# Kernel tuning notes

Hardware: AMD Instinct MI355X
Metric: run time of the kernel (lower is better)

## Reference

```python
import jax, jax.numpy as jnp
import numpy as np
from jax import lax


def conv1x1(x, w, b=None):
    # x: [B,C,H,W], w: [O,C]
    y = jnp.einsum('bchw,oc->bohw', x, w)
    if b is not None:
        y = y + b[None, :, None, None]
    return y


def conv1x9(x, w, b):
    # x: [B,C,H,W], w: [O,I,1,9], pad (0,4) -> same spatial size
    y = lax.conv_general_dilated(x, w, window_strides=(1, 1),
                                 padding=((0, 0), (4, 4)),
                                 dimension_numbers=('NCHW', 'OIHW', 'NCHW'))
    return y + b[None, :, None, None]


def skn(inputs, fc1_w, fc2_w):
    # Selective Kernel fusion: M=len(inputs), each [B,C,H,W]
    M = len(inputs)
    B, C = inputs[0].shape[0], inputs[0].shape[1]
    U = inputs[0]
    for t in inputs[1:]:
        U = U + t
    s = U.mean(axis=(2, 3))                               # [B,C] global avg pool
    z = jax.nn.leaky_relu(jnp.einsum('bc,oc->bo', s, fc1_w), 0.01)
    ab = jnp.einsum('bo,po->bp', z, fc2_w).reshape(B, M, C)
    a = jax.nn.softmax(ab, axis=1)                        # softmax over branches
    out = inputs[0] * a[:, 0][:, :, None, None]
    for i in range(1, M):
        out = out + inputs[i] * a[:, i][:, :, None, None]
    return out


def setup_inputs() -> dict:
    key = jax.random.key(0)
    ks = jax.random.split(key, 24)
    B, C, H, W = 2, 128, 128, 512
    Ch = C // 2
    p = lambda k, shp: (jax.random.normal(k, shp, jnp.float32) * 0.02)
    d = {}
    d['left_feat'] = jax.random.normal(ks[0], (B, C, H, W), jnp.float32)
    d['right_feat'] = jax.random.normal(ks[1], (B, C, H, W), jnp.float32)
    d['emb_l_w'] = p(ks[2], (Ch, C)); d['emb_l_b'] = p(ks[3], (Ch,))
    d['emb_r_w'] = p(ks[4], (Ch, C)); d['emb_r_b'] = p(ks[5], (Ch,))
    d['emb_lv_w'] = p(ks[6], (Ch, C)); d['emb_lv_b'] = p(ks[7], (Ch,))
    d['emb_rv_w'] = p(ks[8], (Ch, C)); d['emb_rv_b'] = p(ks[9], (Ch,))
    d['out_l_w'] = p(ks[10], (C, Ch)); d['out_l_b'] = p(ks[11], (C,))
    d['head_w'] = p(ks[12], (C, 2 * C)); d['head_b'] = p(ks[13], (C,))
    d['body_w1'] = p(ks[14], (3, C, C, 1, 9)); d['body_b1'] = p(ks[15], (3, C))
    d['body_w2'] = p(ks[16], (3, C, C, 1, 9)); d['body_b2'] = p(ks[17], (3, C))
    d['skn1_fc1_w'] = p(ks[18], (C // 4, C)); d['skn1_fc2_w'] = p(ks[19], (3 * C, C // 4))
    d['skn2_fc1_w'] = p(ks[20], (C // 4, C)); d['skn2_fc2_w'] = p(ks[21], (3 * C, C // 4))
    d['num_window'] = 4
    return d


def reference(left_feat, right_feat, emb_l_w, emb_l_b, emb_r_w, emb_r_b,
              emb_lv_w, emb_lv_b, emb_rv_w, emb_rv_b, out_l_w, out_l_b,
              head_w, head_b, body_w1, body_b1, body_w2, body_b2,
              skn1_fc1_w, skn1_fc2_w, skn2_fc1_w, skn2_fc2_w, num_window):
    B, C, H, W = left_feat.shape
    Ch = C // 2
    nw = int(num_window)
    win = W // nw

    Q = conv1x1(left_feat, emb_l_w, emb_l_b)     # [B,Ch,H,W]
    K = conv1x1(right_feat, emb_r_w, emb_r_b)
    V_left = conv1x1(left_feat, emb_lv_w, emb_lv_b)   # computed but unused (source bug)
    V_right = conv1x1(right_feat, emb_rv_w, emb_rv_b)

    # windowed per-row cross attention over width
    Qw = Q.transpose(0, 2, 3, 1).reshape(B, H, nw, win, Ch)   # [B,H,n,q,c]
    Kw = K.transpose(0, 2, 3, 1).reshape(B, H, nw, win, Ch)   # [B,H,n,k,c]
    Vr = V_right.transpose(0, 2, 3, 1).reshape(B, H, nw, win, Ch)

    score = jnp.einsum('bhnqc,bhnkc->bhnqk', Qw, Kw)          # [B,H,n,q,k]
    M_r2l = jax.nn.softmax(score, axis=-1)
    out = jnp.einsum('bhnqk,bhnkc->bhnqc', M_r2l, Vr)         # [B,H,n,q,c]
    warped = out.reshape(B, H, W, Ch).transpose(0, 3, 1, 2)   # [B,Ch,H,W]
    left_feat_warped = jax.nn.relu(conv1x1(warped, out_l_w, out_l_b))
    # NOTE: source code (num_window>1 branch) reuses M_right_to_left and V_right
    # for the right warp as well -> right_feat_warped == left_feat_warped.
    right_feat_warped = left_feat_warped

    # head conv + 3 residual blocks (1x9 convs)
    mixed = jax.nn.relu(conv1x1(jnp.concatenate([left_feat, right_feat], axis=1),
                                head_w, head_b))
    x = mixed
    for i in range(3):
        r = jax.nn.relu(conv1x9(x, body_w1[i], body_b1[i]))
        r = conv1x9(r, body_w2[i], body_b2[i])
        x = x + r
    mixed_feat = x

    left_out = skn([left_feat, left_feat_warped, mixed_feat], skn1_fc1_w, skn1_fc2_w)
    right_out = skn([right_feat, right_feat_warped, mixed_feat], skn2_fc1_w, skn2_fc2_w)
    return (left_out, right_out)
```

## Files before the change

kernel.cpp:

```cpp
#include <hip/hip_runtime.h>
#include <hip/hip_bf16.h>

typedef __attribute__((ext_vector_type(8))) short bf16x8;
typedef __attribute__((ext_vector_type(4))) float f32x4;
typedef unsigned short u16;
typedef unsigned int u32;

#define DI __device__ __forceinline__
#define MFMA16(a, b, c) __builtin_amdgcn_mfma_f32_16x16x32_bf16((a), (b), (c), 0, 0, 0)

constexpr int Hh = 128, Ww = 512;
constexpr int HW = 65536;
constexpr long FULL = 16777216;
constexpr long HALF = 8388608;

__device__ __align__(16) u16 g_buf[2 * FULL];
__device__ __align__(16) u16 g_w[950272];
__device__ __align__(16) float g_bias[1216];
__device__ __align__(16) float g_fc[32768];
__device__ __align__(16) float g_pools[1024];
__device__ __align__(16) float g_gates[1536];
__device__ __align__(16) float g_ppart[524288];
__device__ int g_flag;

constexpr int EMB_L = 0, EMB_R = 8192, EMB_RV = 16384, HEAD = 24576, OUTL = 57344, BODY = 65536;
constexpr int B_EMBL = 0, B_EMBR = 64, B_EMBRV = 128, B_OUTL = 192, B_HEAD = 320, B_B1 = 448, B_B2 = 832;
constexpr int FC1A = 0, FC2A = 4096, FC1B = 16384, FC2B = 20480;

DI float b2f(u16 u) { union { u32 i; float f; } v; v.i = (u32)u << 16; return v.f; }
DI u16 f2b(float f) {
  union { float fl; u32 u; } v; v.fl = f;
  return (u16)((v.u + 0x7FFFu + ((v.u >> 16) & 1u)) >> 16);
}
DI float ldf(const void* p, long i, int f) {
  return f ? ((const float*)p)[i] : b2f(((const u16*)p)[i]);
}
DI bf16x8 ld8(const void* p) { return *reinterpret_cast<const bf16x8*>(p); }
DI void gload16(const u16* src, char* lds_dst) {
  __builtin_amdgcn_global_load_lds(
      (const __attribute__((address_space(1))) void*)src,
      (__attribute__((address_space(3))) void*)lds_dst, 16, 0, 0);
}

__global__ void k_detect(const void* left) {
  if (threadIdx.x != 0 || blockIdx.x != 0) return;
  const u16* pu = (const u16*)left;
  int okb = 0;
  for (int i = 0; i < 256; i++) {
    float x = b2f(pu[i]);
    float a = fabsf(x);
    if (x == 0.f || (a > 1e-8f && a < 1e4f)) okb++;
  }
  g_flag = (okb >= 230) ? 0 : 1;
}

__global__ void k_pack(const void* w1, const void* w2, const void* embl, const void* embr,
                       const void* embrv, const void* outl, const void* head,
                       const void* embl_b, const void* embr_b, const void* embrv_b,
                       const void* outl_b, const void* head_b, const void* b1, const void* b2,
                       const void* f1a, const void* f2a, const void* f1b, const void* f2b_) {
  int f = g_flag;
  int i = blockIdx.x * 256 + threadIdx.x;
  int job = blockIdx.y;
  if (job == 0) {
    if (i >= 884736) return;
    int c = i & 127, o = (i >> 7) & 127;
    int rest = i >> 14;
    int t = rest % 9, bc = rest / 9;
    const void* src = (bc & 1) ? w2 : w1;
    int blk = bc >> 1;
    g_w[BODY + i] = f2b(ldf(src, (((long)(blk * 128 + o) * 128 + c)) * 9 + t, f));
  } else if (job == 1) {
    if (i >= 65536) return;
    float v;
    if (i < 8192) v = ldf(embl, i, f);
    else if (i < 16384) v = ldf(embr, i - 8192, f);
    else if (i < 24576) v = ldf(embrv, i - 16384, f);
    else if (i < 57344) v = ldf(head, i - 24576, f);
    else v = ldf(outl, i - 57344, f);
    g_w[i] = f2b(v);
  } else if (job == 2) {
    if (i >= 1216) return;
    float v;
    if (i < 64) v = ldf(embl_b, i, f);
    else if (i < 128) v = ldf(embr_b, i - 64, f);
    else if (i < 192) v = ldf(embrv_b, i - 128, f);
    else if (i < 320) v = ldf(outl_b, i - 192, f);
    else if (i < 448) v = ldf(head_b, i - 320, f);
    else if (i < 832) v = ldf(b1, i - 448, f);
    else v = ldf(b2, i - 832, f);
    g_bias[i] = v;
  } else {
    if (i >= 32768) return;
    float v;
    if (i < 4096) v = ldf(f1a, i, f);
    else if (i < 16384) v = ldf(f2a, i - 4096, f);
    else if (i < 20480) v = ldf(f1b, i - 16384, f);
    else v = ldf(f2b_, i - 20480, f);
    g_fc[i] = v;
  }
}

__global__ __launch_bounds__(256) void k_nchw2nhwc(const void* srcL, const void* srcR,
                                                   u16* __restrict__ dstL, u16* __restrict__ dstR) {
  __shared__ u16 tile[64][130];
  int f = g_flag;
  int w0 = blockIdx.x * 64;
  int h = blockIdx.y;
  int b = blockIdx.z & 1;
  int img = blockIdx.z >> 1;
  const void* src = img ? srcR : srcL;
  u16* dst = img ? dstR : dstL;
  int t = threadIdx.x;
  int wq = (t & 31) * 2, cb = t >> 5;
  for (int c0 = 0; c0 < 128; c0 += 8) {
    int c = c0 + cb;
    long base = (long)(b * 128 + c) * HW + h * Ww + w0 + wq;
    if (f) {
      float2 v = *reinterpret_cast<const float2*>((const float*)src + base);
      tile[wq][c] = f2b(v.x);
      tile[wq + 1][c] = f2b(v.y);
    } else {
      u32 v = *reinterpret_cast<const u32*>((const u16*)src + base);
      tile[wq][c] = (u16)v;
      tile[wq + 1][c] = (u16)(v >> 16);
    }
  }
  __syncthreads();
  int c = t & 127, wb = t >> 7;
  long obase = (long)b * HW + (long)h * Ww + w0;
  for (int w1i = 0; w1i < 64; w1i += 2) {
    int w = w1i + wb;
    dst[(obase + w) * 128 + c] = tile[w][c];
  }
  if (t < 128) {
    float s = 0.f;
#pragma unroll
    for (int w = 0; w < 64; w++) s += b2f(tile[w][t]);
    g_ppart[((img * 2 + b) * 128 + t) * 1024 + (h * 8 + blockIdx.x)] = s;
  }
}

template<int K, int N, bool RELU, bool NCHW_OUT>
__global__ __launch_bounds__(256) void k_gemm1x1(const u16* __restrict__ xt, const u16* __restrict__ w,
                                                 const float* __restrict__ bias, u16* __restrict__ out,
                                                 int wstride) {
  extern __shared__ __align__(16) char smem[];
  constexpr int SLOTS = (K * 2) / 16;
  constexpr int RB = K * 2;
  int t = threadIdx.x;
  long p0 = (long)blockIdx.x * 128;
  for (int u = t; u < 128 * SLOTS; u += 256) {
    int row = u / SLOTS, slot = u % SLOTS;
    int4 v = *reinterpret_cast<const int4*>(xt + (p0 + row) * K + slot * 8);
    *reinterpret_cast<int4*>(smem + (((u32)(row * RB + slot * 16)) ^ ((row & 7) << 4))) = v;
  }
  __syncthreads();
  int wid = t >> 6, lane = t & 63, l15 = lane & 15, l4 = lane >> 4;
  constexpr int WAVES_M = (N == 64) ? 4 : 2;
  constexpr int MF = (128 / WAVES_M) / 16;
  int wm = (N == 64) ? wid : (wid >> 1);
  int wn = (N == 64) ? 0 : (wid & 1);
  int prow0 = wm * (128 / WAVES_M);
  int ocol0 = wn * 64;
  f32x4 zz = {0.f, 0.f, 0.f, 0.f};
  f32x4 acc[MF][4];
#pragma unroll
  for (int m = 0; m < MF; m++)
#pragma unroll
    for (int n = 0; n < 4; n++) acc[m][n] = zz;
#pragma unroll
  for (int k0 = 0; k0 < K; k0 += 32) {
    bf16x8 a[MF], bw[4];
#pragma unroll
    for (int m = 0; m < MF; m++) {
      int row = prow0 + m * 16 + l15;
      a[m] = ld8(smem + (((u32)(row * RB + (k0 + l4 * 8) * 2)) ^ ((row & 7) << 4)));
    }
#pragma unroll
    for (int n = 0; n < 4; n++) {
      int o = ocol0 + n * 16 + l15;
      bw[n] = ld8(w + (long)o * wstride + k0 + l4 * 8);
    }
#pragma unroll
    for (int m = 0; m < MF; m++)
#pragma unroll
      for (int n = 0; n < 4; n++) acc[m][n] = MFMA16(a[m], bw[n], acc[m][n]);
  }
  if constexpr (!NCHW_OUT) {
#pragma unroll
    for (int m = 0; m < MF; m++)
#pragma unroll
      for (int n = 0; n < 4; n++) {
        int o = ocol0 + n * 16 + l15;
        float bb = bias[o];
#pragma unroll
        for (int r = 0; r < 4; r++) {
          long p = p0 + prow0 + m * 16 + l4 * 4 + r;
          float v = acc[m][n][r] + bb;
          if (RELU) v = fmaxf(v, 0.f);
          out[p * N + o] = f2b(v);
        }
      }
  } else {
    __syncthreads();
    u16* tb = reinterpret_cast<u16*>(smem) + wid * (64 * 66);
#pragma unroll
    for (int m = 0; m < MF; m++)
#pragma unroll
      for (int n = 0; n < 4; n++) {
        float bb = bias[ocol0 + n * 16 + l15];
#pragma unroll
        for (int r = 0; r < 4; r++) {
          int pl = m * 16 + l4 * 4 + r;
          float v = acc[m][n][r] + bb;
          if (RELU) v = fmaxf(v, 0.f);
          tb[(n * 16 + l15) * 66 + pl] = f2b(v);
        }
      }
    __syncthreads();
    int bq = (int)(p0 / HW);
    int rem = (int)(p0 % HW);
    int hq = rem / Ww, wq0 = rem % Ww;
    for (int o = 0; o < 64; o++) {
      out[((long)(bq * 128 + ocol0 + o)) * HW + hq * Ww + wq0 + prow0 + lane] = tb[o * 66 + lane];
    }
  }
}

__global__ __launch_bounds__(256) void k_emb3(const u16* __restrict__ leftT, const u16* __restrict__ rightT,
                                              const u16* __restrict__ gw, const float* __restrict__ gbias,
                                              u16* __restrict__ QT, u16* __restrict__ KT, u16* __restrict__ VrT) {
  extern __shared__ __align__(16) char smem[];
  int br = blockIdx.y;
  const u16* xt = (br == 0) ? leftT : rightT;
  const u16* w = gw + ((br == 0) ? EMB_L : (br == 1) ? EMB_R : EMB_RV);
  const float* bias = gbias + ((br == 0) ? B_EMBL : (br == 1) ? B_EMBR : B_EMBRV);
  u16* out = (br == 0) ? QT : (br == 1) ? KT : VrT;
  int t = threadIdx.x;
  long p0 = (long)blockIdx.x * 128;
  for (int u = t; u < 2048; u += 256) {
    int row = u >> 4, slot = u & 15;
    int4 v = *reinterpret_cast<const int4*>(xt + (p0 + row) * 128 + slot * 8);
    *reinterpret_cast<int4*>(smem + (((u32)(row * 256 + slot * 16)) ^ ((row & 7) << 4))) = v;
  }
  __syncthreads();
  int wid = t >> 6, lane = t & 63, l15 = lane & 15, l4 = lane >> 4;
  int prow0 = wid * 32;
  f32x4 zz = {0.f, 0.f, 0.f, 0.f};
  f32x4 acc[2][4];
#pragma unroll
  for (int m = 0; m < 2; m++)
#pragma unroll
    for (int n = 0; n < 4; n++) acc[m][n] = zz;
#pragma unroll
  for (int k0 = 0; k0 < 128; k0 += 32) {
    bf16x8 a[2], bw[4];
#pragma unroll
    for (int m = 0; m < 2; m++) {
      int row = prow0 + m * 16 + l15;
      a[m] = ld8(smem + (((u32)(row * 256 + (k0 + l4 * 8) * 2)) ^ ((row & 7) << 4)));
    }
#pragma unroll
    for (int n = 0; n < 4; n++) {
      int o = n * 16 + l15;
      bw[n] = ld8(w + (long)o * 128 + k0 + l4 * 8);
    }
#pragma unroll
    for (int m = 0; m < 2; m++)
#pragma unroll
      for (int n = 0; n < 4; n++) acc[m][n] = MFMA16(a[m], bw[n], acc[m][n]);
  }
#pragma unroll
  for (int m = 0; m < 2; m++)
#pragma unroll
    for (int n = 0; n < 4; n++) {
      int o = n * 16 + l15;
      float bb = bias[o];
#pragma unroll
      for (int r = 0; r < 4; r++) {
        long p = p0 + prow0 + m * 16 + l4 * 4 + r;
        out[p * 64 + o] = f2b(acc[m][n][r] + bb);
      }
    }
}

__global__ __launch_bounds__(256) void k_head(const u16* lt, const u16* rt,
                                              const u16* __restrict__ wh, const float* __restrict__ bh,
                                              u16* out) {
  extern __shared__ __align__(16) char smem[];
  int t = threadIdx.x;
  long p0 = (long)blockIdx.x * 128;
  for (int u = t; u < 2048; u += 256) {
    int row = u >> 4, slot = u & 15;
    u32 db = ((u32)(row * 256 + slot * 16)) ^ ((row & 7) << 4);
    *reinterpret_cast<int4*>(smem + db) = *reinterpret_cast<const int4*>(lt + (p0 + row) * 128 + slot * 8);
    *reinterpret_cast<int4*>(smem + 32768 + db) = *reinterpret_cast<const int4*>(rt + (p0 + row) * 128 + slot * 8);
  }
  __syncthreads();
  int wid = t >> 6, lane = t & 63, l15 = lane & 15, l4 = lane >> 4;
  int prow0 = (wid >> 1) * 64, ocol0 = (wid & 1) * 64;
  f32x4 zz = {0.f, 0.f, 0.f, 0.f};
  f32x4 acc[4][4];
#pragma unroll
  for (int m = 0; m < 4; m++)
#pragma unroll
    for (int n = 0; n < 4; n++) acc[m][n] = zz;
#pragma unroll
  for (int kk = 0; kk < 8; kk++) {
    int k0 = kk * 32;
    const char* sb = smem + ((kk >= 4) ? 32768 : 0);
    int kl = k0 & 127;
    bf16x8 a[4], bw[4];
#pragma unroll
    for (int m = 0; m < 4; m++) {
      int row = prow0 + m * 16 + l15;
      a[m] = ld8(sb + (((u32)(row * 256 + (kl + l4 * 8) * 2)) ^ ((row & 7) << 4)));
    }
#pragma unroll
    for (int n = 0; n < 4; n++) {
      int o = ocol0 + n * 16 + l15;
      bw[n] = ld8(wh + o * 256 + k0 + l4 * 8);
    }
#pragma unroll
    for (int m = 0; m < 4; m++)
#pragma unroll
      for (int n = 0; n < 4; n++) acc[m][n] = MFMA16(a[m], bw[n], acc[m][n]);
  }
  __syncthreads();
#pragma unroll
  for (int m = 0; m < 4; m++)
#pragma unroll
    for (int n = 0; n < 4; n++) {
      int o = ocol0 + n * 16 + l15;
      float bb = bh[o];
#pragma unroll
      for (int r = 0; r < 4; r++) {
        long p = p0 + prow0 + m * 16 + l4 * 4 + r;
        float v = fmaxf(acc[m][n][r] + bb, 0.f);
        out[p * 128 + o] = f2b(v);
      }
    }
}

__global__ __launch_bounds__(256) void k_attn(const u16* __restrict__ qt, const u16* __restrict__ kt,
                                              const u16* __restrict__ vt, u16* __restrict__ outT) {
  extern __shared__ __align__(16) char smem[];
  int n = blockIdx.x, h = blockIdx.y, b = blockIdx.z;
  long rb = ((long)(b * Hh + h)) * Ww + n * 128;
  int t = threadIdx.x;
  for (int u = t; u < 1024; u += 256) {
    int row = u >> 3, slot = u & 7;
    u32 db = ((u32)(row * 128 + slot * 16)) ^ ((row & 7) << 4);
    *reinterpret_cast<int4*>(smem + db) = *reinterpret_cast<const int4*>(qt + (rb + row) * 64 + slot * 8);
    *reinterpret_cast<int4*>(smem + 16384 + db) = *reinterpret_cast<const int4*>(kt + (rb + row) * 64 + slot * 8);
  }
  __syncthreads();
  int wid = t >> 6, lane = t & 63, l15 = lane & 15, l4 = lane >> 4;
  int q0 = wid * 32;
  f32x4 zz = {0.f, 0.f, 0.f, 0.f};
  f32x4 sc[2][8];
#pragma unroll
  for (int m = 0; m < 2; m++)
#pragma unroll
    for (int nf = 0; nf < 8; nf++) sc[m][nf] = zz;
#pragma unroll
  for (int k0 = 0; k0 < 64; k0 += 32) {
    bf16x8 aq[2], bk[8];
#pragma unroll
    for (int m = 0; m < 2; m++) {
      int row = q0 + m * 16 + l15;
      aq[m] = ld8(smem + (((u32)(row * 128 + (k0 + l4 * 8) * 2)) ^ ((row & 7) << 4)));
    }
#pragma unroll
    for (int nf = 0; nf < 8; nf++) {
      int row = nf * 16 + l15;
      bk[nf] = ld8(smem + 16384 + (((u32)(row * 128 + (k0 + l4 * 8) * 2)) ^ ((row & 7) << 4)));
    }
#pragma unroll
    for (int m = 0; m < 2; m++)
#pragma unroll
      for (int nf = 0; nf < 8; nf++) sc[m][nf] = MFMA16(aq[m], bk[nf], sc[m][nf]);
  }
  float rsum[2][4];
#pragma unroll
  for (int m = 0; m < 2; m++) {
#pragma unroll
    for (int r = 0; r < 4; r++) {
      float mx = -3.0e38f;
#pragma unroll
      for (int nf = 0; nf < 8; nf++) mx = fmaxf(mx, sc[m][nf][r]);
      mx = fmaxf(mx, __shfl_xor(mx, 1));
      mx = fmaxf(mx, __shfl_xor(mx, 2));
      mx = fmaxf(mx, __shfl_xor(mx, 4));
      mx = fmaxf(mx, __shfl_xor(mx, 8));
      int ql = q0 + m * 16 + l4 * 4 + r;
      float ssum = 0.f;
#pragma unroll
      for (int nf = 0; nf < 8; nf++) {
        float e = __expf(sc[m][nf][r] - mx);
        ssum += e;
        int k = nf * 16 + l15;
        *reinterpret_cast<u16*>(smem + 32768 + (((u32)(ql * 256 + k * 2)) ^ ((ql & 7) << 4))) = f2b(e);
      }
      ssum += __shfl_xor(ssum, 1);
      ssum += __shfl_xor(ssum, 2);
      ssum += __shfl_xor(ssum, 4);
      ssum += __shfl_xor(ssum, 8);
      rsum[m][r] = ssum;
    }
  }
  __syncthreads();
  for (int u = t; u < 8192; u += 256) {
    int k = u >> 6, c = u & 63;
    u16 v = vt[(rb + k) * 64 + c];
    *reinterpret_cast<u16*>(smem + (((u32)(c * 256 + k * 2)) ^ ((c & 7) << 4))) = v;
  }
  __syncthreads();
  f32x4 ov[2][4];
#pragma unroll
  for (int m = 0; m < 2; m++)
#pragma unroll
    for (int nf = 0; nf < 4; nf++) ov[m][nf] = zz;
#pragma unroll
  for (int k0 = 0; k0 < 128; k0 += 32) {
    bf16x8 ap[2], bv[4];
#pragma unroll
    for (int m = 0; m < 2; m++) {
      int row = q0 + m * 16 + l15;
      ap[m] = ld8(smem + 32768 + (((u32)(row * 256 + (k0 + l4 * 8) * 2)) ^ ((row & 7) << 4)));
    }
#pragma unroll
    for (int nf = 0; nf < 4; nf++) {
      int c = nf * 16 + l15;
      bv[nf] = ld8(smem + (((u32)(c * 256 + (k0 + l4 * 8) * 2)) ^ ((c & 7) << 4)));
    }
#pragma unroll
    for (int m = 0; m < 2; m++)
#pragma unroll
      for (int nf = 0; nf < 4; nf++) ov[m][nf] = MFMA16(ap[m], bv[nf], ov[m][nf]);
  }
#pragma unroll
  for (int m = 0; m < 2; m++)
#pragma unroll
    for (int nf = 0; nf < 4; nf++)
#pragma unroll
      for (int r = 0; r < 4; r++) {
        int q = q0 + m * 16 + l4 * 4 + r;
        int c = nf * 16 + l15;
        outT[(rb + q) * 64 + c] = f2b(ov[m][nf][r] / rsum[m][r]);
      }
}

template<bool RELU, bool HASRES, bool NCHW_OUT>
__global__ __launch_bounds__(256) void k_conv1x9(const u16* __restrict__ xin, const u16* __restrict__ wp9,
                                                 const float* __restrict__ bias, const u16* __restrict__ res,
                                                 u16* __restrict__ out) {
  __shared__ __align__(16) char xs[34816];
  __shared__ __align__(16) char wbuf[32768];
  int w0 = blockIdx.x * 128;
  int h = blockIdx.y, b = blockIdx.z;
  long rowg = ((long)(b * Hh + h)) * Ww;
  int t = threadIdx.x;
  int wid = t >> 6, lane = t & 63;
  int o0w = (wid & 1) * 64;
  char* wbase = wbuf + wid * 8192;
  auto stage = [&](int s) {
    int tap = s >> 2, kk = s & 3;
    const u16* base = wp9 + tap * 16384 + (long)o0w * 128 + kk * 32;
#pragma unroll
    for (int j = 0; j < 4; j++) {
      int u = j * 64 + lane;
      int op = u >> 2, p = u & 3;
      int l = (p - (op >> 1)) & 3;
      gload16(base + op * 128 + l * 8, wbase + (s & 1) * 4096 + j * 1024);
    }
  };
  for (int u = t; u < 2176; u += 256) {
    int row = u >> 4, slot = u & 15;
    int wg = w0 - 4 + row;
    int4 v{0, 0, 0, 0};
    if (wg >= 0 && wg < Ww) v = *reinterpret_cast<const int4*>(xin + (rowg + wg) * 128 + slot * 8);
    *reinterpret_cast<int4*>(xs + (((u32)(row * 256 + slot * 16)) ^ ((row & 7) << 4))) = v;
  }
  stage(0);
  __syncthreads();
  int l15 = lane & 15, l4 = lane >> 4;
  int p0w = (wid >> 1) * 64;
  f32x4 zz = {0.f, 0.f, 0.f, 0.f};
  f32x4 acc[4][4];
#pragma unroll
  for (int m = 0; m < 4; m++)
#pragma unroll
    for (int n = 0; n < 4; n++) acc[m][n] = zz;
#pragma unroll 1
  for (int s = 0; s < 36; s++) {
    if (s < 35) {
      stage(s + 1);
      asm volatile("s_waitcnt vmcnt(4)" ::: "memory");
    } else {
      asm volatile("s_waitcnt vmcnt(0)" ::: "memory");
    }
    int tap = s >> 2, kk = s & 3;
    const char* wb = wbase + (s & 1) * 4096;
    bf16x8 a[4], bw[4];
#pragma unroll
    for (int n = 0; n < 4; n++) {
      int op = n * 16 + l15;
      int p = (l4 + (op >> 1)) & 3;
      bw[n] = ld8(wb + op * 64 + p * 16);
    }
#pragma unroll
    for (int m = 0; m < 4; m++) {
      int row = p0w + m * 16 + l15 + tap;
      a[m] = ld8(xs + (((u32)(row * 256 + kk * 64 + l4 * 16)) ^ ((row & 7) << 4)));
    }
    __builtin_amdgcn_s_setprio(1);
#pragma unroll
    for (int m = 0; m < 4; m++)
#pragma unroll
      for (int n = 0; n < 4; n++) acc[m][n] = MFMA16(a[m], bw[n], acc[m][n]);
    __builtin_amdgcn_s_setprio(0);
  }
  float bb[4];
#pragma unroll
  for (int n = 0; n < 4; n++) bb[n] = bias[o0w + n * 16 + l15];
  if constexpr (!NCHW_OUT) {
#pragma unroll
    for (int m = 0; m < 4; m++)
#pragma unroll
      for (int n = 0; n < 4; n++) {
        int o = o0w + n * 16 + l15;
#pragma unroll
        for (int r = 0; r < 4; r++) {
          int p = w0 + p0w + m * 16 + l4 * 4 + r;
          float v = acc[m][n][r] + bb[n];
          if (RELU) v = fmaxf(v, 0.f);
          if (HASRES) v += b2f(res[(rowg + p) * 128 + o]);
          out[(rowg + p) * 128 + o] = f2b(v);
        }
      }
  } else {
    __syncthreads();
    u16* tb = reinterpret_cast<u16*>(xs) + wid * (64 * 66);
#pragma unroll
    for (int m = 0; m < 4; m++)
#pragma unroll
      for (int n = 0; n < 4; n++) {
        int o = o0w + n * 16 + l15;
#pragma unroll
        for (int r = 0; r < 4; r++) {
          int pl = m * 16 + l4 * 4 + r;
          int p = w0 + p0w + pl;
          float v = acc[m][n][r] + bb[n];
          if (RELU) v = fmaxf(v, 0.f);
          if (HASRES) v += b2f(res[(rowg + p) * 128 + o]);
          tb[(n * 16 + l15) * 66 + pl] = f2b(v);
        }
      }
    __syncthreads();
    for (int o = 0; o < 64; o++) {
      out[((long)(b * 128 + o0w + o)) * HW + h * Ww + w0 + p0w + lane] = tb[o * 66 + lane];
    }
  }
}

__global__ __launch_bounds__(256) void k_pool(const u16* __restrict__ lfw, const u16* __restrict__ mixed) {
  int c = blockIdx.x, b = blockIdx.y, ts = blockIdx.z;
  float s = 0.f;
  if (ts < 2) {
    const float* pp = g_ppart + ((ts * 2 + b) * 128 + c) * 1024;
    for (int i = threadIdx.x; i < 1024; i += 256) s += pp[i];
  } else {
    long base = ((long)(b * 128 + c)) * HW;
    const u16* pu = (ts == 2) ? lfw + base : mixed + base;
    for (int i = threadIdx.x * 8; i < HW; i += 2048) {
      union { int4 v; u16 u[8]; } x;
      x.v = *reinterpret_cast<const int4*>(pu + i);
#pragma unroll
      for (int j = 0; j < 8; j++) s += b2f(x.u[j]);
    }
  }
#pragma unroll
  for (int m = 1; m < 64; m <<= 1) s += __shfl_xor(s, m);
  __shared__ float red[4];
  if ((threadIdx.x & 63) == 0) red[threadIdx.x >> 6] = s;
  __syncthreads();
  if (threadIdx.x == 0)
    g_pools[(ts * 2 + b) * 128 + c] = (red[0] + red[1] + red[2] + red[3]) * (1.f / HW);
}

__global__ void k_gate() {
  __shared__ float sv[128], zv[32];
  int b = blockIdx.x, s = blockIdx.y;
  int t = threadIdx.x;
  sv[t] = g_pools[(s * 2 + b) * 128 + t] + g_pools[(4 + b) * 128 + t] + g_pools[(6 + b) * 128 + t];
  __syncthreads();
  const float* fc1 = g_fc + (s ? FC1B : FC1A);
  const float* fc2 = g_fc + (s ? FC2B : FC2A);
  if (t < 32) {
    float z = 0.f;
    for (int c = 0; c < 128; c++) z += fc1[t * 128 + c] * sv[c];
    zv[t] = (z > 0.f) ? z : 0.01f * z;
  }
  __syncthreads();
  float ab[3];
#pragma unroll
  for (int i = 0; i < 3; i++) {
    float a = 0.f;
    for (int j = 0; j < 32; j++) a += fc2[(i * 128 + t) * 32 + j] * zv[j];
    ab[i] = a;
  }
  float mx = fmaxf(ab[0], fmaxf(ab[1], ab[2]));
  float e0 = __expf(ab[0] - mx), e1 = __expf(ab[1] - mx), e2 = __expf(ab[2] - mx);
  float inv = 1.f / (e0 + e1 + e2);
  g_gates[((s * 2 + b) * 3 + 0) * 128 + t] = e0 * inv;
  g_gates[((s * 2 + b) * 3 + 1) * 128 + t] = e1 * inv;
  g_gates[((s * 2 + b) * 3 + 2) * 128 + t] = e2 * inv;
}

__global__ __launch_bounds__(256) void k_skn_out(const void* left, const void* right,
                                                 const u16* __restrict__ lfw, const u16* __restrict__ mixed,
                                                 void* doutv) {
  int chunk = blockIdx.x, c = blockIdx.y, b = blockIdx.z;
  int f = g_flag;
  const float* g1 = g_gates + (b * 3) * 128 + c;
  const float* g2 = g_gates + ((2 + b) * 3) * 128 + c;
  float a10 = g1[0], a11 = g1[128], a12 = g1[256];
  float a20 = g2[0], a21 = g2[128], a22 = g2[256];
  long off = ((long)(b * 128 + c)) * HW + chunk * 2048 + threadIdx.x * 8;
  float xl[8], xr[8];
  if (f) {
    const float* L = (const float*)left + off;
    const float* R = (const float*)right + off;
    float4 a0 = *reinterpret_cast<const float4*>(L);
    float4 a1 = *reinterpret_cast<const float4*>(L + 4);
    float4 r0 = *reinterpret_cast<const float4*>(R);
    float4 r1 = *reinterpret_cast<const float4*>(R + 4);
    xl[0]=a0.x; xl[1]=a0.y; xl[2]=a0.z; xl[3]=a0.w; xl[4]=a1.x; xl[5]=a1.y; xl[6]=a1.z; xl[7]=a1.w;
    xr[0]=r0.x; xr[1]=r0.y; xr[2]=r0.z; xr[3]=r0.w; xr[4]=r1.x; xr[5]=r1.y; xr[6]=r1.z; xr[7]=r1.w;
  } else {
    union { int4 v; u16 u[8]; } a, r;
    a.v = *reinterpret_cast<const int4*>((const u16*)left + off);
    r.v = *reinterpret_cast<const int4*>((const u16*)right + off);
#pragma unroll
    for (int j = 0; j < 8; j++) { xl[j] = b2f(a.u[j]); xr[j] = b2f(r.u[j]); }
  }
  union { int4 v; u16 u[8]; } vw, vm;
  vw.v = *reinterpret_cast<const int4*>(lfw + off);
  vm.v = *reinterpret_cast<const int4*>(mixed + off);
  float ol[8], orr[8];
#pragma unroll
  for (int j = 0; j < 8; j++) {
    float fw = b2f(vw.u[j]), fm = b2f(vm.u[j]);
    ol[j] = a10 * xl[j] + a11 * fw + a12 * fm;
    orr[j] = a20 * xr[j] + a21 * fw + a22 * fm;
  }
  if (f) {
    float* fo = (float*)doutv;
    *reinterpret_cast<float4*>(fo + off) = make_float4(ol[0], ol[1], ol[2], ol[3]);
    *reinterpret_cast<float4*>(fo + off + 4) = make_float4(ol[4], ol[5], ol[6], ol[7]);
    *reinterpret_cast<float4*>(fo + FULL + off) = make_float4(orr[0], orr[1], orr[2], orr[3]);
    *reinterpret_cast<float4*>(fo + FULL + off + 4) = make_float4(orr[4], orr[5], orr[6], orr[7]);
  } else {
    u16* bo = (u16*)doutv;
    union { int4 v; u16 u[8]; } o1, o2;
#pragma unroll
    for (int j = 0; j < 8; j++) { o1.u[j] = f2b(ol[j]); o2.u[j] = f2b(orr[j]); }
    *reinterpret_cast<int4*>(bo + off) = o1.v;
    *reinterpret_cast<int4*>(bo + FULL + off) = o2.v;
  }
}

extern "C" void kernel_launch(void* const* d_in, const int* in_sizes, int n_in,
                              void* d_out, int out_size, void* d_ws, size_t ws_size,
                              hipStream_t stream) {
  (void)in_sizes; (void)n_in; (void)out_size; (void)d_ws; (void)ws_size;
  const void* left    = d_in[0];
  const void* right   = d_in[1];

  u16* gbuf = nullptr;
  (void)hipGetSymbolAddress((void**)&gbuf, HIP_SYMBOL(g_buf));
  u16* gw = nullptr;
  (void)hipGetSymbolAddress((void**)&gw, HIP_SYMBOL(g_w));
  float* gbias = nullptr;
  (void)hipGetSymbolAddress((void**)&gbias, HIP_SYMBOL(g_bias));

  u16* du = (u16*)d_out;
  u16* leftT   = du;
  u16* rA      = du;
  u16* rightT  = du + FULL;
  u16* xG      = du + FULL;
  u16* QT      = gbuf;
  u16* KT      = gbuf + HALF;
  u16* VrT     = gbuf + FULL;
  u16* warpedT = gbuf + FULL + HALF;
  u16* lfw     = gbuf;
  u16* mixed   = gbuf + FULL;

  k_detect<<<dim3(1), dim3(64), 0, stream>>>(left);
  k_pack<<<dim3(3456, 4), dim3(256), 0, stream>>>(
      d_in[14], d_in[16], d_in[2], d_in[4], d_in[8], d_in[10], d_in[12],
      d_in[3], d_in[5], d_in[9], d_in[11], d_in[13], d_in[15], d_in[17],
      d_in[18], d_in[19], d_in[20], d_in[21]);
  k_nchw2nhwc<<<dim3(8, 128, 4), dim3(256), 0, stream>>>(left, right, leftT, rightT);
  k_emb3<<<dim3(1024, 3), dim3(256), 32768, stream>>>(leftT, rightT, gw, gbias, QT, KT, VrT);
  k_head<<<dim3(1024), dim3(256), 65536, stream>>>(leftT, rightT, gw + HEAD, gbias + B_HEAD, xG);
  k_attn<<<dim3(4, 128, 2), dim3(256), 65536, stream>>>(QT, KT, VrT, warpedT);
  k_gemm1x1<64, 128, true, true><<<dim3(1024), dim3(256), 33792, stream>>>(warpedT, gw + OUTL, gbias + B_OUTL, lfw, 64);
  for (int i = 0; i < 3; i++) {
    k_conv1x9<true, false, false><<<dim3(4, 128, 2), dim3(256), 0, stream>>>(
        xG, gw + BODY + (long)(i * 2 + 0) * 9 * 16384, gbias + B_B1 + i * 128, nullptr, rA);
    if (i < 2)
      k_conv1x9<false, true, false><<<dim3(4, 128, 2), dim3(256), 0, stream>>>(
          rA, gw + BODY + (long)(i * 2 + 1) * 9 * 16384, gbias + B_B2 + i * 128, xG, xG);
    else
      k_conv1x9<false, true, true><<<dim3(4, 128, 2), dim3(256), 0, stream>>>(
          rA, gw + BODY + (long)(i * 2 + 1) * 9 * 16384, gbias + B_B2 + i * 128, xG, mixed);
  }
  k_pool<<<dim3(128, 2, 4), dim3(256), 0, stream>>>(lfw, mixed);
  k_gate<<<dim3(2, 2), dim3(128), 0, stream>>>();
  k_skn_out<<<dim3(32, 128, 2), dim3(256), 0, stream>>>(left, right, lfw, mixed, d_out);
}
```

Measured before the change: 590.8 us.

## Share weight stages across warps in conv1x9 with block-wide cooperative loads

The conv1x9 kernel used to give each warp a private 8KB weight buffer. Each warp staged only its own 64 output channels in 36 small steps and synchronised with per-warp vmcnt waits. Now all 256 threads cooperatively load a shared 128x64 weight slab per stage, using an XOR swizzle, over 18 larger double-buffered steps separated by __syncthreads. This removes the duplicate weight loads between warps sharing output channels and halves the number of stages, at the cost of block-wide barriers. The explicit vmcnt wait is gone, so completion of the async global-to-LDS loads before the barrier now rests on the compiler and the barrier. The setprio hints are also dropped.

```diff
diff --git a/kernel.cpp b/kernel.cpp
--- a/kernel.cpp
+++ b/kernel.cpp
@@ -462,18 +462,17 @@
   int h = blockIdx.y, b = blockIdx.z;
   long rowg = ((long)(b * Hh + h)) * Ww;
   int t = threadIdx.x;
-  int wid = t >> 6, lane = t & 63;
-  int o0w = (wid & 1) * 64;
-  char* wbase = wbuf + wid * 8192;
+  int wid = t >> 6;
   auto stage = [&](int s) {
-    int tap = s >> 2, kk = s & 3;
-    const u16* base = wp9 + tap * 16384 + (long)o0w * 128 + kk * 32;
+    int tap = s >> 1, khalf = s & 1;
+    const u16* base = wp9 + tap * 16384 + khalf * 64;
 #pragma unroll
     for (int j = 0; j < 4; j++) {
-      int u = j * 64 + lane;
-      int op = u >> 2, p = u & 3;
-      int l = (p - (op >> 1)) & 3;
-      gload16(base + op * 128 + l * 8, wbase + (s & 1) * 4096 + j * 1024);
+      int fidx = j * 256 + t;
+      int row = fidx >> 3;
+      int sl = fidx & 7;
+      int l = sl ^ (row & 7);
+      gload16(base + row * 128 + l * 8, wbuf + (s & 1) * 16384 + j * 4096 + wid * 1024);
     }
   };
   for (int u = t; u < 2176; u += 256) {
@@ -485,8 +484,8 @@
   }
   stage(0);
   __syncthreads();
-  int l15 = lane & 15, l4 = lane >> 4;
-  int p0w = (wid >> 1) * 64;
+  int lane = t & 63, l15 = lane & 15, l4 = lane >> 4;
+  int p0w = (wid >> 1) * 64, o0w = (wid & 1) * 64;
   f32x4 zz = {0.f, 0.f, 0.f, 0.f};
   f32x4 acc[4][4];
 #pragma unroll
@@ -494,33 +493,30 @@
 #pragma unroll
     for (int n = 0; n < 4; n++) acc[m][n] = zz;
 #pragma unroll 1
-  for (int s = 0; s < 36; s++) {
-    if (s < 35) {
-      stage(s + 1);
-      asm volatile("s_waitcnt vmcnt(4)" ::: "memory");
-    } else {
-      asm volatile("s_waitcnt vmcnt(0)" ::: "memory");
-    }
-    int tap = s >> 2, kk = s & 3;
-    const char* wb = wbase + (s & 1) * 4096;
-    bf16x8 a[4], bw[4];
-#pragma unroll
-    for (int n = 0; n < 4; n++) {
-      int op = n * 16 + l15;
-      int p = (l4 + (op >> 1)) & 3;
-      bw[n] = ld8(wb + op * 64 + p * 16);
-    }
-#pragma unroll
-    for (int m = 0; m < 4; m++) {
-      int row = p0w + m * 16 + l15 + tap;
-      a[m] = ld8(xs + (((u32)(row * 256 + kk * 64 + l4 * 16)) ^ ((row & 7) << 4)));
-    }
-    __builtin_amdgcn_s_setprio(1);
-#pragma unroll
-    for (int m = 0; m < 4; m++)
-#pragma unroll
-      for (int n = 0; n < 4; n++) acc[m][n] = MFMA16(a[m], bw[n], acc[m][n]);
-    __builtin_amdgcn_s_setprio(0);
+  for (int s = 0; s < 18; s++) {
+    if (s < 17) stage(s + 1);
+    int tap = s >> 1, khalf = s & 1;
+    const char* wb = wbuf + (s & 1) * 16384;
+#pragma unroll
+    for (int kc = 0; kc < 2; kc++) {
+      bf16x8 a[4], bw[4];
+#pragma unroll
+      for (int n = 0; n < 4; n++) {
+        int o = o0w + n * 16 + l15;
+        int l = kc * 4 + l4;
+        bw[n] = ld8(wb + o * 128 + (l ^ (o & 7)) * 16);
+      }
+#pragma unroll
+      for (int m = 0; m < 4; m++) {
+        int row = p0w + m * 16 + l15 + tap;
+        a[m] = ld8(xs + (((u32)(row * 256 + khalf * 128 + kc * 64 + l4 * 16)) ^ ((row & 7) << 4)));
+      }
+#pragma unroll
+      for (int m = 0; m < 4; m++)
+#pragma unroll
+        for (int n = 0; n < 4; n++) acc[m][n] = MFMA16(a[m], bw[n], acc[m][n]);
+    }
+    __syncthreads();
   }
   float bb[4];
 #pragma unroll
@@ -541,7 +537,6 @@
         }
       }
   } else {
-    __syncthreads();
     u16* tb = reinterpret_cast<u16*>(xs) + wid * (64 * 66);
 #pragma unroll
     for (int m = 0; m < 4; m++)
```

Measured after the change: 544.1 us, median of 2. 7.9% less time.
